# Kernel optimization log

Hardware: AMD Instinct MI355X
Metric: run time of the kernel (lower is better)

## Reference

```python
import jax, jax.numpy as jnp
from jax import lax
import numpy as np


def _tv1d_row(y, lam):
    """Condat's direct O(n) 1D TV-L1 prox (TV1D_denoise) on one row.
    Solves min_x 0.5*||x-y||^2 + lam * sum|x_{i+1}-x_i|.
    State machine translation of Condat (2013) Algorithm 1.
    """
    W = y.shape[0]
    idx = jnp.arange(W)
    dt = y.dtype

    def write(out, lo, hi, v):
        # out[lo:hi+1] = v  (masked, jit-friendly)
        return jnp.where((idx >= lo) & (idx <= hi), v, out)

    def cond_fn(s):
        return ~s[9]

    def body_fn(s):
        out, k, k0, km, kp, umin, umax, vmin, vmax, done = s
        T = jnp.array(True)
        F = jnp.array(False)

        def branchA(_):  # k == W-1
            def a1(_):  # umin < 0: flush negative segment at vmin
                o = write(out, k0, km, vmin)
                k0n = km + 1
                vminn = y[jnp.minimum(k0n, W - 1)]
                return (o, k0n, k0n, k0n, kp, lam, vminn + lam - vmax, vminn, vmax, F)

            def a2(_):  # umax > 0: flush positive segment at vmax
                o = write(out, k0, kp, vmax)
                k0n = kp + 1
                vmaxn = y[jnp.minimum(k0n, W - 1)]
                return (o, k0n, k0n, km, k0n, vmaxn - lam - vmin, -lam, vmin, vmaxn, F)

            def a3(_):  # terminate
                v = vmin + umin / (k - k0 + 1).astype(dt)
                o = write(out, k0, k, v)
                return (o, k, k0, km, kp, umin, umax, v, vmax, T)

            return lax.cond(umin < 0, a1,
                            lambda _: lax.cond(umax > 0, a2, a3, None), None)

        def branchB(_):  # k < W-1
            yn = y[jnp.minimum(k + 1, W - 1)]
            umin_t = umin + yn - vmin
            umax_t = umax + yn - vmax

            def b1(_):  # negative jump: flush at vmin, restart
                o = write(out, k0, km, vmin)
                k0n = km + 1
                vminn = y[jnp.minimum(k0n, W - 1)]
                return (o, k0n, k0n, k0n, k0n, lam, -lam, vminn, vminn + 2 * lam, F)

            def b2(_):  # positive jump: flush at vmax, restart
                o = write(out, k0, kp, vmax)
                k0n = kp + 1
                vmaxn = y[jnp.minimum(k0n, W - 1)]
                return (o, k0n, k0n, k0n, k0n, lam, -lam, vmaxn - 2 * lam, vmaxn, F)

            def b3(_):  # extend current segment
                kn = k + 1
                denom = (kn - k0 + 1).astype(dt)
                hit_min = umin_t >= lam
                hit_max = umax_t <= -lam
                vminn = jnp.where(hit_min, vmin + (umin_t - lam) / denom, vmin)
                uminn = jnp.where(hit_min, lam, umin_t)
                kmn = jnp.where(hit_min, kn, km)
                vmaxn = jnp.where(hit_max, vmax + (umax_t + lam) / denom, vmax)
                umaxn = jnp.where(hit_max, -lam, umax_t)
                kpn = jnp.where(hit_max, kn, kp)
                return (out, kn, k0, kmn, kpn, uminn, umaxn, vminn, vmaxn, F)

            return lax.cond(umin_t < -lam, b1,
                            lambda _: lax.cond(umax_t > lam, b2, b3, None), None)

        return lax.cond(k == W - 1, branchA, branchB, None)

    z = jnp.int32(0)
    init = (jnp.zeros_like(y), z, z, z, z, lam, -lam, y[0] - lam, y[0] + lam, jnp.array(False))
    return lax.while_loop(cond_fn, body_fn, init)[0]


def tv1d_batch(y_flat, lam_rows):
    return jax.vmap(_tv1d_row)(y_flat, lam_rows)


def setup_inputs() -> dict:
    key = jax.random.key(0)
    N, C, H, W = 8, 3, 256, 512
    y = jax.random.normal(key, (N, C, H, W), dtype=jnp.float32)
    # learned lmbd parameter initialized so that softplus(lmbd) = 0.5 (lmbd_init=0.5, lmbd_zero<0 -> offset 0)
    lmbd = jnp.full((1, C), float(np.log(np.expm1(0.5))), dtype=jnp.float32)
    return {"y": y, "lmbd": lmbd}


def reference(y, lmbd):
    N, C, H, W = y.shape
    lam = jax.nn.softplus(lmbd)  # get_lmbd_val with lmbd_offset = 0
    lam_rows = jnp.broadcast_to(lam.reshape(1, C, 1), (N, C, H)).reshape(-1)  # (N*C*H,)
    x = tv1d_batch(y.reshape(-1, W), lam_rows)
    return x.reshape(N, C, H, W)
```

## Files before the change

### kernel.cpp

```cpp
#include <hip/hip_runtime.h>
#include <math.h>

#define TVW 512
#define TVH 256
#define TVC 3
#define WPB 2
#define BLOCK (WPB * 64)
#define PADF 128

__global__ __launch_bounds__(BLOCK)
void tv1d_condat_wave_kernel(const float* __restrict__ y,
                             const float* __restrict__ lmbd,
                             float* __restrict__ out,
                             int total_rows) {
    __shared__ __align__(16) float buf[WPB * TVW + PADF];
    const int tid  = threadIdx.x;
    const int wave = tid >> 6;
    const int lane = tid & 63;
    const int l32  = lane & 31;
    const bool hi  = lane >= 32;
    const int row  = blockIdx.x * WPB + wave;

#define RLF(SRC, IDX) __uint_as_float(__builtin_amdgcn_readlane(__float_as_uint(SRC), (IDX)))

    if (row < total_rows) {
        {
            const float4* s4 = (const float4*)(y + (size_t)row * TVW);
            float4* b4 = (float4*)(buf + wave * TVW);
            #pragma unroll
            for (int i = 0; i < TVW / 4; i += 64)
                b4[i + lane] = s4[i + lane];
        }

        const int c = (row / TVH) % TVC;
        float lam = log1pf(expf(lmbd[c]));
        lam = __uint_as_float(__builtin_amdgcn_readfirstlane(__float_as_uint(lam)));
        const float nlam   = -lam;
        const float twolam = 2.0f * lam;
        float* x = buf + wave * TVW;

        const float sgn   = hi ? -1.0f : 1.0f;
        const float vnlam = -lam;
        const float vmcn  = hi ? -twolam : -0.0f;
        const float vmcp  = hi ? -0.0f : -twolam;
        const float laneF = (float)lane;
        const float rw0c  = __builtin_amdgcn_rcpf(laneF + 1.0f);
        const float rw1c  = __builtin_amdgcn_rcpf(laneF + 57.0f);

        int k0, wb, trips, trips_rel, s_ji, seg_guard, kmv, kcv;
        unsigned long long jb;
        float u, v, nvs, wv, tt, denbF, rwin, rwin2, ywin, ywin2;
        bool negj;

        k0 = 0; seg_guard = 4096; jb = 0;
        ywin  = x[lane];
        ywin2 = x[56 + lane];
        nvs = RLF(ywin, 0);
        v = fmaf(sgn, nvs, vnlam);
        u = lam;
        kmv = 0; kcv = 1;

#define TVSTEP(SY, SR) { \
            const float u_t = fmaf(sgn, (SY), u) - v; \
            jb = __ballot(u_t < nlam);    \
            if (jb) goto midjump; \
            kmv = (u_t >= lam) ? kcv : kmv;   \
            kcv += 1; \
            const float u_n = fminf(u_t, lam); \
            v = fmaf(u_t - u_n, (SR), v);     \
            u = u_n; }

#define TVSLIDE() { \
            ywin = ywin2; \
            wb += 56; \
            ywin2 = x[wb + 56 + lane]; \
            s_ji -= 56; trips_rel -= 56; \
            rwin = rwin2; \
            rwin2 = __builtin_amdgcn_rcpf(laneF + denbF); \
            denbF += 56.0f; }

seg_start:
        if (--seg_guard < 0) goto done;
        trips = (TVW - 1) - k0;
        trips_rel = trips;
        wb = k0;
        s_ji = 1;
        denbF = 113.0f;
        rwin = rw0c; rwin2 = rw1c;
        if (trips >= 8) {
            TVSTEP(RLF(ywin, 1), 0.5f)
            TVSTEP(RLF(ywin, 2), (1.0f / 3.0f))
            TVSTEP(RLF(ywin, 3), 0.25f)
            TVSTEP(RLF(ywin, 4), 0.2f)
            TVSTEP(RLF(ywin, 5), (1.0f / 6.0f))
            TVSTEP(RLF(ywin, 6), (1.0f / 7.0f))
            TVSTEP(RLF(ywin, 7), 0.125f)
            TVSTEP(RLF(ywin, 8), (1.0f / 9.0f))
            s_ji = 9;
            for (;;) {
                if (s_ji + 7 > trips_rel) break;
                if (s_ji > 56) TVSLIDE()
                {
                    const int j0 = s_ji,     j1 = s_ji + 1, j2 = s_ji + 2, j3 = s_ji + 3,
                              j4 = s_ji + 4, j5 = s_ji + 5, j6 = s_ji + 6, j7 = s_ji + 7;
                    const float y0 = RLF(ywin, j0), y1 = RLF(ywin, j1),
                                y2 = RLF(ywin, j2), y3 = RLF(ywin, j3),
                                y4 = RLF(ywin, j4), y5 = RLF(ywin, j5),
                                y6 = RLF(ywin, j6), y7 = RLF(ywin, j7);
                    const float r0 = RLF(rwin, j0), r1 = RLF(rwin, j1),
                                r2 = RLF(rwin, j2), r3 = RLF(rwin, j3),
                                r4 = RLF(rwin, j4), r5 = RLF(rwin, j5),
                                r6 = RLF(rwin, j6), r7 = RLF(rwin, j7);
                    TVSTEP(y0, r0) TVSTEP(y1, r1) TVSTEP(y2, r2) TVSTEP(y3, r3)
                    TVSTEP(y4, r4) TVSTEP(y5, r5) TVSTEP(y6, r6) TVSTEP(y7, r7)
                }
                s_ji += 8;
            }
        }
        while (s_ji <= trips_rel) {
            if (s_ji > 63) TVSLIDE()
            TVSTEP(RLF(ywin, s_ji), RLF(rwin, s_ji))
            s_ji += 1;
        }

        {
            const unsigned long long bb = __ballot(u < 0.0f);
            if ((unsigned)bb) {
                const int fe = __builtin_amdgcn_readlane(kmv, 0);
                const int k0n = fe + 1;
                wv = v;
                if (k0n < TVW) {
                    ywin  = x[k0n + lane];
                    ywin2 = x[k0n + 56 + lane];
                }
                { const int pe = fe < TVW - 1 ? fe : TVW - 1;
                  if (!hi) for (int p = k0 + l32; p <= pe; p += 32) x[p] = wv; }
                if (k0n >= TVW) goto done;
                nvs = RLF(ywin, 0);
                tt = fmaf(sgn, nvs, vnlam);
                u = hi ? (tt - v) : lam;
                v = hi ? v : nvs;
                kmv = hi ? kmv : k0n;
                kcv = k0n + 1;
                k0 = k0n;
                goto seg_start;
            } else if ((unsigned)(bb >> 32)) {
                const int fe = __builtin_amdgcn_readlane(kmv, 32);
                const int k0n = fe + 1;
                wv = -v;
                if (k0n < TVW) {
                    ywin  = x[k0n + lane];
                    ywin2 = x[k0n + 56 + lane];
                }
                { const int pe = fe < TVW - 1 ? fe : TVW - 1;
                  if (hi) for (int p = k0 + l32; p <= pe; p += 32) x[p] = wv; }
                if (k0n >= TVW) goto done;
                nvs = RLF(ywin, 0);
                tt = nvs + vnlam;
                u = hi ? lam : (tt - v);
                v = hi ? (-nvs) : v;
                kmv = hi ? k0n : kmv;
                kcv = k0n + 1;
                k0 = k0n;
                goto seg_start;
            } else {
                const float vt = fmaf(u, __builtin_amdgcn_rcpf((float)(trips + 1)), v);
                if (!hi) for (int p = k0 + l32; p < TVW; p += 32) x[p] = vt;
                goto done;
            }
        }

midjump:
        {
            negj = (unsigned)jb != 0;
            const int fe = __builtin_amdgcn_readlane(kmv, negj ? 0 : 32);
            const int k0n = fe + 1;
            wv = hi ? -v : v;
            ywin  = x[k0n + lane];
            ywin2 = x[k0n + 56 + lane];
            {
                const int p0 = k0 + l32;
                if ((negj != hi) && (p0 <= fe)) x[p0] = wv;
                if (fe - k0 >= 32) {
                    if (negj != hi)
                        for (int p = p0 + 32; p <= fe; p += 32) x[p] = wv;
                }
            }
            nvs = RLF(ywin, 0);
            v = fmaf(sgn, nvs, negj ? vmcn : vmcp);
            u = lam;
            kmv = k0n; kcv = k0n + 1;
            k0 = k0n;
            goto seg_start;
        }
#undef TVSTEP
#undef TVSLIDE
done:   ;
        {
            const float4* b4 = (const float4*)(buf + wave * TVW);
            float4* d4 = (float4*)(out + (size_t)row * TVW);
            #pragma unroll
            for (int i = 0; i < TVW / 4; i += 64)
                d4[i + lane] = b4[i + lane];
        }
    }
#undef RLF
}

extern "C" void kernel_launch(void* const* d_in, const int* in_sizes, int n_in,
                              void* d_out, int out_size, void* d_ws, size_t ws_size,
                              hipStream_t stream) {
    const float* y    = (const float*)d_in[0];
    const float* lmbd = (const float*)d_in[1];
    float* out = (float*)d_out;

    const int total_rows = in_sizes[0] / TVW;
    const int grid = (total_rows + WPB - 1) / WPB;
    tv1d_condat_wave_kernel<<<grid, BLOCK, 0, stream>>>(y, lmbd, out, total_rows);
}
```

Before: 243.7 us.

## Batch jump ballots over groups of four steps with checkpoint and replay

Takes the per-step ballot and branch out of the inner Condat loop. It runs four steps without branching, tracks the minimum u_t, and issues one ballot per group. If any lane detected a jump, state is restored from a checkpoint and the group is replayed step by step with the original branching step. The unrolled group shrinks from 8 to 4 and the special first-8 prologue is dropped. Rows with frequent jumps pay the cost of replay.

```diff
diff --git a/kernel.cpp b/kernel.cpp
--- a/kernel.cpp
+++ b/kernel.cpp
@@ -48,8 +48,10 @@
         const float rw1c  = __builtin_amdgcn_rcpf(laneF + 57.0f);
 
         int k0, wb, trips, trips_rel, s_ji, seg_guard, kmv, kcv;
+        int kms, kcs, rp_end;
         unsigned long long jb;
         float u, v, nvs, wv, tt, denbF, rwin, rwin2, ywin, ywin2;
+        float us, vs, fm;
         bool negj;
 
         k0 = 0; seg_guard = 4096; jb = 0;
@@ -70,6 +72,15 @@
             v = fmaf(u_t - u_n, (SR), v);     \
             u = u_n; }
 
+#define TVSTEP_NB(SY, SR) { \
+            const float u_t = fmaf(sgn, (SY), u) - v; \
+            fm = fminf(fm, u_t); \
+            kmv = (u_t >= lam) ? kcv : kmv; \
+            kcv += 1; \
+            const float u_n = fminf(u_t, lam); \
+            v = fmaf(u_t - u_n, (SR), v); \
+            u = u_n; }
+
 #define TVSLIDE() { \
             ywin = ywin2; \
             wb += 56; \
@@ -87,42 +98,44 @@
         s_ji = 1;
         denbF = 113.0f;
         rwin = rw0c; rwin2 = rw1c;
-        if (trips >= 8) {
-            TVSTEP(RLF(ywin, 1), 0.5f)
-            TVSTEP(RLF(ywin, 2), (1.0f / 3.0f))
-            TVSTEP(RLF(ywin, 3), 0.25f)
-            TVSTEP(RLF(ywin, 4), 0.2f)
-            TVSTEP(RLF(ywin, 5), (1.0f / 6.0f))
-            TVSTEP(RLF(ywin, 6), (1.0f / 7.0f))
-            TVSTEP(RLF(ywin, 7), 0.125f)
-            TVSTEP(RLF(ywin, 8), (1.0f / 9.0f))
-            s_ji = 9;
-            for (;;) {
-                if (s_ji + 7 > trips_rel) break;
-                if (s_ji > 56) TVSLIDE()
-                {
-                    const int j0 = s_ji,     j1 = s_ji + 1, j2 = s_ji + 2, j3 = s_ji + 3,
-                              j4 = s_ji + 4, j5 = s_ji + 5, j6 = s_ji + 6, j7 = s_ji + 7;
-                    const float y0 = RLF(ywin, j0), y1 = RLF(ywin, j1),
-                                y2 = RLF(ywin, j2), y3 = RLF(ywin, j3),
-                                y4 = RLF(ywin, j4), y5 = RLF(ywin, j5),
-                                y6 = RLF(ywin, j6), y7 = RLF(ywin, j7);
-                    const float r0 = RLF(rwin, j0), r1 = RLF(rwin, j1),
-                                r2 = RLF(rwin, j2), r3 = RLF(rwin, j3),
-                                r4 = RLF(rwin, j4), r5 = RLF(rwin, j5),
-                                r6 = RLF(rwin, j6), r7 = RLF(rwin, j7);
-                    TVSTEP(y0, r0) TVSTEP(y1, r1) TVSTEP(y2, r2) TVSTEP(y3, r3)
-                    TVSTEP(y4, r4) TVSTEP(y5, r5) TVSTEP(y6, r6) TVSTEP(y7, r7)
-                }
-                s_ji += 8;
-            }
+group_loop:
+        for (;;) {
+            if (s_ji + 3 > trips_rel) break;
+            if (s_ji > 60) TVSLIDE()
+            us = u; vs = v; kms = kmv; kcs = kcv;
+            fm = 1.0e30f;
+            {
+                const int j0 = s_ji, j1 = s_ji + 1, j2 = s_ji + 2, j3 = s_ji + 3;
+                const float y0 = RLF(ywin, j0), y1 = RLF(ywin, j1),
+                            y2 = RLF(ywin, j2), y3 = RLF(ywin, j3);
+                const float r0 = RLF(rwin, j0), r1 = RLF(rwin, j1),
+                            r2 = RLF(rwin, j2), r3 = RLF(rwin, j3);
+                TVSTEP_NB(y0, r0) TVSTEP_NB(y1, r1)
+                TVSTEP_NB(y2, r2) TVSTEP_NB(y3, r3)
+            }
+            jb = __ballot(fm < nlam);
+            if (jb) {
+                u = us; v = vs; kmv = kms; kcv = kcs;
+                rp_end = s_ji + 4;
+                goto replay;
+            }
+            s_ji += 4;
         }
         while (s_ji <= trips_rel) {
             if (s_ji > 63) TVSLIDE()
             TVSTEP(RLF(ywin, s_ji), RLF(rwin, s_ji))
             s_ji += 1;
         }
-
+        goto boundary;
+
+replay:
+        while (s_ji < rp_end) {
+            TVSTEP(RLF(ywin, s_ji), RLF(rwin, s_ji))
+            s_ji += 1;
+        }
+        goto group_loop;
+
+boundary:
         {
             const unsigned long long bb = __ballot(u < 0.0f);
             if ((unsigned)bb) {
@@ -194,6 +207,7 @@
             goto seg_start;
         }
 #undef TVSTEP
+#undef TVSTEP_NB
 #undef TVSLIDE
 done:   ;
         {
```

Measured after the change: 371.4 us. 1.52x slower.

## Reuse sliding y window across segment restarts instead of reloading from LDS

Applied to the files above, without the earlier changes.

Replaces the per-segment reload of the y window at the new start index with a persistent window that advances in fixed 56-element strides, so a restart after a jump reads from registers rather than reissuing two LDS loads and waiting on them. The unrolled 8-step inner loop and the precomputed reciprocal window are dropped in favour of a simple per-step loop that reads reciprocals from a lane-indexed register for the first 63 steps and computes rcp inline afterwards. This shortens the serial latency on each segment restart but loses the unrolled readlane batching, so long segments may run slower per step.

```diff
diff --git a/kernel.cpp b/kernel.cpp
--- a/kernel.cpp
+++ b/kernel.cpp
@@ -44,21 +44,22 @@
         const float vmcn  = hi ? -twolam : -0.0f;
         const float vmcp  = hi ? -0.0f : -twolam;
         const float laneF = (float)lane;
-        const float rw0c  = __builtin_amdgcn_rcpf(laneF + 1.0f);
-        const float rw1c  = __builtin_amdgcn_rcpf(laneF + 57.0f);
+        const float rwc   = __builtin_amdgcn_rcpf(laneF + 1.0f);
 
-        int k0, wb, trips, trips_rel, s_ji, seg_guard, kmv, kcv;
+        int k0, wb, dw2, j, jm, jend, rd, kmv, kcv, seg_guard;
         unsigned long long jb;
-        float u, v, nvs, wv, tt, denbF, rwin, rwin2, ywin, ywin2;
+        float u, v, nvs, wv, tt, rdf, ywin, ywin2;
         bool negj;
 
-        k0 = 0; seg_guard = 4096; jb = 0;
+        k0 = 0; wb = 0; dw2 = 56; seg_guard = 6144; jb = 0;
         ywin  = x[lane];
         ywin2 = x[56 + lane];
         nvs = RLF(ywin, 0);
         v = fmaf(sgn, nvs, vnlam);
         u = lam;
         kmv = 0; kcv = 1;
+        j = 1; rd = 1;
+        jend = TVW - 1 - wb;
 
 #define TVSTEP(SY, SR) { \
             const float u_t = fmaf(sgn, (SY), u) - v; \
@@ -70,101 +71,74 @@
             v = fmaf(u_t - u_n, (SR), v);     \
             u = u_n; }
 
-#define TVSLIDE() { \
-            ywin = ywin2; \
-            wb += 56; \
-            ywin2 = x[wb + 56 + lane]; \
-            s_ji -= 56; trips_rel -= 56; \
-            rwin = rwin2; \
-            rwin2 = __builtin_amdgcn_rcpf(laneF + denbF); \
-            denbF += 56.0f; }
-
-seg_start:
-        if (--seg_guard < 0) goto done;
-        trips = (TVW - 1) - k0;
-        trips_rel = trips;
-        wb = k0;
-        s_ji = 1;
-        denbF = 113.0f;
-        rwin = rw0c; rwin2 = rw1c;
-        if (trips >= 8) {
-            TVSTEP(RLF(ywin, 1), 0.5f)
-            TVSTEP(RLF(ywin, 2), (1.0f / 3.0f))
-            TVSTEP(RLF(ywin, 3), 0.25f)
-            TVSTEP(RLF(ywin, 4), 0.2f)
-            TVSTEP(RLF(ywin, 5), (1.0f / 6.0f))
-            TVSTEP(RLF(ywin, 6), (1.0f / 7.0f))
-            TVSTEP(RLF(ywin, 7), 0.125f)
-            TVSTEP(RLF(ywin, 8), (1.0f / 9.0f))
-            s_ji = 9;
-            for (;;) {
-                if (s_ji + 7 > trips_rel) break;
-                if (s_ji > 56) TVSLIDE()
-                {
-                    const int j0 = s_ji,     j1 = s_ji + 1, j2 = s_ji + 2, j3 = s_ji + 3,
-                              j4 = s_ji + 4, j5 = s_ji + 5, j6 = s_ji + 6, j7 = s_ji + 7;
-                    const float y0 = RLF(ywin, j0), y1 = RLF(ywin, j1),
-                                y2 = RLF(ywin, j2), y3 = RLF(ywin, j3),
-                                y4 = RLF(ywin, j4), y5 = RLF(ywin, j5),
-                                y6 = RLF(ywin, j6), y7 = RLF(ywin, j7);
-                    const float r0 = RLF(rwin, j0), r1 = RLF(rwin, j1),
-                                r2 = RLF(rwin, j2), r3 = RLF(rwin, j3),
-                                r4 = RLF(rwin, j4), r5 = RLF(rwin, j5),
-                                r6 = RLF(rwin, j6), r7 = RLF(rwin, j7);
-                    TVSTEP(y0, r0) TVSTEP(y1, r1) TVSTEP(y2, r2) TVSTEP(y3, r3)
-                    TVSTEP(y4, r4) TVSTEP(y5, r5) TVSTEP(y6, r6) TVSTEP(y7, r7)
-                }
-                s_ji += 8;
+loopA:
+        jm = jend < 63 ? jend : 63;
+        while (j <= jm) {
+            TVSTEP(RLF(ywin, j), RLF(rwc, rd))
+            j += 1; rd += 1;
+        }
+        if (j > jend) goto boundary;
+        rdf = (float)(rd + 1);
+        while (j <= jend) {
+            if (j - dw2 >= 64) {
+                dw2 += 56;
+                ywin2 = x[wb + dw2 + lane];
             }
-        }
-        while (s_ji <= trips_rel) {
-            if (s_ji > 63) TVSLIDE()
-            TVSTEP(RLF(ywin, s_ji), RLF(rwin, s_ji))
-            s_ji += 1;
+            TVSTEP(RLF(ywin2, j - dw2), __builtin_amdgcn_rcpf(rdf))
+            j += 1; rd += 1; rdf += 1.0f;
         }
 
+boundary:
         {
             const unsigned long long bb = __ballot(u < 0.0f);
             if ((unsigned)bb) {
                 const int fe = __builtin_amdgcn_readlane(kmv, 0);
                 const int k0n = fe + 1;
                 wv = v;
-                if (k0n < TVW) {
-                    ywin  = x[k0n + lane];
-                    ywin2 = x[k0n + 56 + lane];
-                }
                 { const int pe = fe < TVW - 1 ? fe : TVW - 1;
                   if (!hi) for (int p = k0 + l32; p <= pe; p += 32) x[p] = wv; }
                 if (k0n >= TVW) goto done;
-                nvs = RLF(ywin, 0);
+                if (dw2 != 56) { ywin2 = x[wb + 56 + lane]; dw2 = 56; }
+                while (k0n - wb >= 56) {
+                    wb += 56;
+                    ywin = ywin2;
+                    ywin2 = x[wb + 56 + lane];
+                }
+                nvs = RLF(ywin, k0n - wb);
                 tt = fmaf(sgn, nvs, vnlam);
                 u = hi ? (tt - v) : lam;
                 v = hi ? v : nvs;
                 kmv = hi ? kmv : k0n;
                 kcv = k0n + 1;
                 k0 = k0n;
-                goto seg_start;
+                j = k0n - wb + 1; rd = 1; jend = TVW - 1 - wb;
+                if (--seg_guard < 0) goto done;
+                goto loopA;
             } else if ((unsigned)(bb >> 32)) {
                 const int fe = __builtin_amdgcn_readlane(kmv, 32);
                 const int k0n = fe + 1;
                 wv = -v;
-                if (k0n < TVW) {
-                    ywin  = x[k0n + lane];
-                    ywin2 = x[k0n + 56 + lane];
-                }
                 { const int pe = fe < TVW - 1 ? fe : TVW - 1;
                   if (hi) for (int p = k0 + l32; p <= pe; p += 32) x[p] = wv; }
                 if (k0n >= TVW) goto done;
-                nvs = RLF(ywin, 0);
+                if (dw2 != 56) { ywin2 = x[wb + 56 + lane]; dw2 = 56; }
+                while (k0n - wb >= 56) {
+                    wb += 56;
+                    ywin = ywin2;
+                    ywin2 = x[wb + 56 + lane];
+                }
+                nvs = RLF(ywin, k0n - wb);
                 tt = nvs + vnlam;
                 u = hi ? lam : (tt - v);
                 v = hi ? (-nvs) : v;
                 kmv = hi ? k0n : kmv;
                 kcv = k0n + 1;
                 k0 = k0n;
-                goto seg_start;
+                j = k0n - wb + 1; rd = 1; jend = TVW - 1 - wb;
+                if (--seg_guard < 0) goto done;
+                goto loopA;
             } else {
-                const float vt = fmaf(u, __builtin_amdgcn_rcpf((float)(trips + 1)), v);
+                const float vt = fmaf(u, __builtin_amdgcn_rcpf((float)(TVW - k0)), v);
                 if (!hi) for (int p = k0 + l32; p < TVW; p += 32) x[p] = vt;
                 goto done;
             }
@@ -176,8 +150,6 @@
             const int fe = __builtin_amdgcn_readlane(kmv, negj ? 0 : 32);
             const int k0n = fe + 1;
             wv = hi ? -v : v;
-            ywin  = x[k0n + lane];
-            ywin2 = x[k0n + 56 + lane];
             {
                 const int p0 = k0 + l32;
                 if ((negj != hi) && (p0 <= fe)) x[p0] = wv;
@@ -186,15 +158,22 @@
                         for (int p = p0 + 32; p <= fe; p += 32) x[p] = wv;
                 }
             }
-            nvs = RLF(ywin, 0);
+            if (dw2 != 56) { ywin2 = x[wb + 56 + lane]; dw2 = 56; }
+            while (k0n - wb >= 56) {
+                wb += 56;
+                ywin = ywin2;
+                ywin2 = x[wb + 56 + lane];
+            }
+            nvs = RLF(ywin, k0n - wb);
             v = fmaf(sgn, nvs, negj ? vmcn : vmcp);
             u = lam;
             kmv = k0n; kcv = k0n + 1;
             k0 = k0n;
-            goto seg_start;
+            j = k0n - wb + 1; rd = 1; jend = TVW - 1 - wb;
+            if (--seg_guard < 0) goto done;
+            goto loopA;
         }
 #undef TVSTEP
-#undef TVSLIDE
 done:   ;
         {
             const float4* b4 = (const float4*)(buf + wave * TVW);
```

New measurement: 331.4 us. +36.0%, slower.
